# Kernel optimization log

Hardware: AMD Instinct MI355X
Metric: run time of the kernel (lower is better)

## Reference

```python
import jax, jax.numpy as jnp
import numpy as np

B, T, DIM = 2, 2048, 1024
N_HEADS, HEAD_DIM, WINDOW = 16, 64, 512
EPS = 0.01


def _rmsnorm(x, gamma, eps):
    # x: [B, T, H*D] float32; normalize over last dim
    rms = jnp.sqrt(jnp.mean(jnp.square(x), axis=-1, keepdims=True) + eps)
    return x / rms * gamma


def setup_inputs() -> dict:
    key = jax.random.key(0)
    ks = jax.random.split(key, 5)
    s = 1.0 / np.sqrt(DIM)
    return {
        "x": jax.random.normal(ks[0], (B, T, DIM), jnp.float32),
        "wq": jax.random.normal(ks[1], (N_HEADS * HEAD_DIM, DIM), jnp.float32) * s,
        "wk": jax.random.normal(ks[2], (N_HEADS * HEAD_DIM, DIM), jnp.float32) * s,
        "wv": jax.random.normal(ks[3], (N_HEADS * HEAD_DIM, DIM), jnp.float32) * s,
        "wo": jax.random.normal(ks[4], (DIM, N_HEADS * HEAD_DIM), jnp.float32) * s,
        "q_gamma": jnp.ones((N_HEADS * HEAD_DIM,), jnp.float32),
        "k_gamma": jnp.ones((N_HEADS * HEAD_DIM,), jnp.float32),
    }


def reference(x, wq, wk, wv, wo, q_gamma, k_gamma):
    Bx, Tx, _ = x.shape
    H, D = N_HEADS, HEAD_DIM
    # projections (Linear with weight [out,in]): [B,T,H*D]
    q = x @ wq.T
    k = x @ wk.T
    v = (x @ wv.T).reshape(Bx, Tx, H, D).transpose(0, 2, 1, 3)  # [B,H,T,D]
    # QK RMSNorm over the flattened H*D dimension (float32 math)
    q = _rmsnorm(q, q_gamma, 1e-6).reshape(Bx, Tx, H, D).transpose(0, 2, 1, 3)
    k = _rmsnorm(k, k_gamma, 1e-6).reshape(Bx, Tx, H, D).transpose(0, 2, 1, 3)
    scale = 1.0 / np.sqrt(D)
    scores = jnp.einsum("bhqd,bhkd->bhqk", q, k) * scale  # [B,H,T,T]
    # ALiBi bias: slopes[h] * (j - i)
    slopes = jnp.asarray([2.0 ** (-8.0 / H * (h + 1)) for h in range(H)], jnp.float32)
    pos = jnp.arange(Tx)
    dist = (pos[None, :] - pos[:, None]).astype(jnp.float32)  # [T,T], dist[i,j]=j-i
    scores = scores + slopes[None, :, None, None] * dist[None, None]
    # causal (j>i) OR beyond sliding window (i-j > window_size)
    j_minus_i = pos[None, :] - pos[:, None]
    mask = (j_minus_i > 0) | (j_minus_i < -WINDOW)
    scores = jnp.where(mask[None, None], -1e9, scores)
    attn = jax.nn.softmax(scores, axis=-1)
    out = jnp.einsum("bhqk,bhkd->bhqd", attn, v)  # [B,H,T,D]
    out = out.transpose(0, 2, 1, 3).reshape(Bx, Tx, H * D)
    return out @ wo.T
```

## Files before the change

kernel.cpp:

```cpp
#include <hip/hip_runtime.h>
#include <stdint.h>

typedef unsigned short u16;
typedef __bf16 bf16x8 __attribute__((ext_vector_type(8)));
typedef float f32x4 __attribute__((ext_vector_type(4)));

#define MFMA16(a, b, c) __builtin_amdgcn_mfma_f32_16x16x32_bf16((a), (b), (c), 0, 0, 0)

__device__ __forceinline__ u16 f2bf(float f) {
  union { float f; uint32_t u; } v; v.f = f;
  uint32_t r = v.u + 0x7fffu + ((v.u >> 16) & 1u);
  return (u16)(r >> 16);
}
__device__ __forceinline__ float bf2f(u16 h) {
  union { uint32_t u; float f; } v; v.u = ((uint32_t)h) << 16;
  return v.f;
}
__device__ __forceinline__ void gload_lds16(const void* g, void* l) {
  __builtin_amdgcn_global_load_lds(
      (const __attribute__((address_space(1))) uint32_t*)(uintptr_t)g,
      (__attribute__((address_space(3))) uint32_t*)(uintptr_t)l, 16, 0, 0);
}
__device__ __forceinline__ uint32_t cvt_pk_bf16(float a, float b) {
  uint32_t r;
  asm("v_cvt_pk_bf16_f32 %0, %1, %2" : "=v"(r) : "v"(a), "v"(b));
  return r;
}

__global__ void k_cvt_all(const float* __restrict__ x, const float* __restrict__ wq,
                          const float* __restrict__ wk, const float* __restrict__ wv,
                          const float* __restrict__ wo, u16* __restrict__ xb,
                          u16* __restrict__ wqb, u16* __restrict__ wkb, u16* __restrict__ wvb,
                          u16* __restrict__ wob) {
  const int i = blockIdx.x * 256 + threadIdx.x;
  const float* src; u16* dst; int off;
  if (i < 1048576)      { src = x;  dst = xb;  off = i; }
  else if (i < 1310720) { src = wq; dst = wqb; off = i - 1048576; }
  else if (i < 1572864) { src = wk; dst = wkb; off = i - 1310720; }
  else if (i < 1835008) { src = wv; dst = wvb; off = i - 1572864; }
  else                  { src = wo; dst = wob; off = i - 1835008; }
  const float4 v = ((const float4*)src)[off];
  u16 o[4] = { f2bf(v.x), f2bf(v.y), f2bf(v.z), f2bf(v.w) };
  *(uint2*)(dst + 4 * (size_t)off) = *(const uint2*)o;
}

template <bool BF16_OUT, int BN>
__device__ __forceinline__ void gemm_core(const u16* __restrict__ A, const u16* __restrict__ Bw,
                                          void* __restrict__ C, int tm, int tn) {
  constexpr int K = 1024, N = 1024, NT = K / 32;
  constexpr int MF = (BN == 128) ? 4 : 2;
  __shared__ __align__(16) u16 As[2][128 * 32];
  __shared__ __align__(16) u16 Bs[2][BN * 32];
  const int tid = threadIdx.x, l = tid & 63, w = tid >> 6;
  const int wm = (BN == 128) ? (w >> 1) * 64 : w * 32;
  const int wn = (BN == 128) ? (w & 1) * 64 : 0;
  const int lo = l & 15, hi8 = (l >> 4) * 8;
  f32x4 acc[MF][4] = {};

  const int srow = l >> 2, scol = (l & 3) * 8;
  const int c0 = w * 2, c1 = w * 2 + 1;
  const u16* Ag0 = A + (size_t)(tm + c0 * 16 + srow) * K + scol;
  const u16* Ag1 = A + (size_t)(tm + c1 * 16 + srow) * K + scol;
  const u16* Bg0 = Bw + (size_t)(tn + c0 * 16 + srow) * K + scol;
  const u16* Bg1 = Bw + (size_t)(tn + c1 * 16 + srow) * K + scol;
  const u16* BgB = Bw + (size_t)(tn + (tid >> 2)) * K + (tid & 3) * 8;

#define STAGE_G(t, buf)                                  \
  {                                                      \
    const int kt_ = (t) * 32;                            \
    gload_lds16(Ag0 + kt_, &As[(buf)][c0 * 512]);        \
    gload_lds16(Ag1 + kt_, &As[(buf)][c1 * 512]);        \
    if constexpr (BN == 128) {                           \
      gload_lds16(Bg0 + kt_, &Bs[(buf)][c0 * 512]);      \
      gload_lds16(Bg1 + kt_, &Bs[(buf)][c1 * 512]);      \
    } else {                                             \
      gload_lds16(BgB + kt_, &Bs[(buf)][tid * 8]);       \
    }                                                    \
  }

  STAGE_G(0, 0);
  STAGE_G(1, 1);

  for (int t = 0; t < NT; ++t) {
    const int cur = t & 1;
    if (t + 1 < NT) {
      if constexpr (BN == 128) asm volatile("s_waitcnt vmcnt(4)");
      else asm volatile("s_waitcnt vmcnt(3)");
    } else {
      asm volatile("s_waitcnt vmcnt(0)");
    }
    __builtin_amdgcn_s_barrier();
    __builtin_amdgcn_sched_barrier(0);

    bf16x8 af[MF], bfr[4];
#pragma unroll
    for (int m = 0; m < MF; ++m) af[m] = *(const bf16x8*)&As[cur][(wm + m * 16 + lo) * 32 + hi8];
#pragma unroll
    for (int n = 0; n < 4; ++n) bfr[n] = *(const bf16x8*)&Bs[cur][(wn + n * 16 + lo) * 32 + hi8];
#pragma unroll
    for (int m = 0; m < MF; ++m)
#pragma unroll
      for (int n = 0; n < 4; ++n) acc[m][n] = MFMA16(af[m], bfr[n], acc[m][n]);

    __builtin_amdgcn_sched_barrier(0);
    __builtin_amdgcn_s_barrier();
    __builtin_amdgcn_sched_barrier(0);
    if (t + 2 < NT) STAGE_G(t + 2, cur);
  }
#undef STAGE_G

  const int r0 = (l >> 4) * 4;
#pragma unroll
  for (int m = 0; m < MF; ++m)
#pragma unroll
    for (int n = 0; n < 4; ++n)
#pragma unroll
      for (int r = 0; r < 4; ++r) {
        const size_t idx = (size_t)(tm + wm + m * 16 + r0 + r) * N + (tn + wn + n * 16 + lo);
        if (BF16_OUT) ((u16*)C)[idx] = f2bf(acc[m][n][r]);
        else ((float*)C)[idx] = acc[m][n][r];
      }
}

__global__ __launch_bounds__(256, 3) void k_gemm_qkv(
    const u16* __restrict__ X, const u16* __restrict__ Wq, const u16* __restrict__ Wk,
    const u16* __restrict__ Wv, u16* __restrict__ Q, u16* __restrict__ Kt, u16* __restrict__ V) {
  const int n = blockIdx.x + (blockIdx.y << 3) + (blockIdx.z << 8);
  const int wid = (n & 7) * 96 + (n >> 3);
  const int bz = wid >> 8, rem = wid & 255, by = rem >> 3, bx = rem & 7;
  const u16* B = bz == 0 ? Wq : bz == 1 ? Wk : Wv;
  u16* C = bz == 0 ? Q : bz == 1 ? Kt : V;
  gemm_core<true, 128>(X, B, C, by * 128, bx * 128);
}
__global__ __launch_bounds__(256, 4) void k_gemm_out(const u16* __restrict__ Ao,
                                                     const u16* __restrict__ Wo,
                                                     float* __restrict__ C) {
  const int n = blockIdx.x + (blockIdx.y << 4);
  const int wid = (n & 7) * 64 + (n >> 3);
  const int by = wid >> 4, bx = wid & 15;
  gemm_core<false, 64>(Ao, Wo, C, by * 128, bx * 64);
}

__global__ __launch_bounds__(256) void k_rmsnorm(u16* __restrict__ Q, u16* __restrict__ Kt,
                                                 const float* __restrict__ qg,
                                                 const float* __restrict__ kg) {
  const int row = blockIdx.x;
  u16* base = (row < 4096) ? (Q + (size_t)row * 1024) : (Kt + (size_t)(row - 4096) * 1024);
  const float* g = (row < 4096) ? qg : kg;
  const int tid = threadIdx.x;
  ushort4 v = ((const ushort4*)base)[tid];
  float f0 = bf2f(v.x), f1 = bf2f(v.y), f2 = bf2f(v.z), f3 = bf2f(v.w);
  float ss = f0 * f0 + f1 * f1 + f2 * f2 + f3 * f3;
#pragma unroll
  for (int off = 32; off >= 1; off >>= 1) ss += __shfl_xor(ss, off, 64);
  __shared__ float wsum[4];
  if ((tid & 63) == 0) wsum[tid >> 6] = ss;
  __syncthreads();
  ss = wsum[0] + wsum[1] + wsum[2] + wsum[3];
  const float rinv = rsqrtf(ss * (1.0f / 1024.0f) + 1e-6f);
  const float4 gv = ((const float4*)g)[tid];
  v.x = f2bf(f0 * rinv * gv.x);
  v.y = f2bf(f1 * rinv * gv.y);
  v.z = f2bf(f2 * rinv * gv.z);
  v.w = f2bf(f3 * rinv * gv.w);
  ((ushort4*)base)[tid] = v;
}

__global__ __launch_bounds__(512, 4) void k_attn(const u16* __restrict__ Q,
                                                 const u16* __restrict__ Kt,
                                                 const u16* __restrict__ V,
                                                 u16* __restrict__ O) {
  constexpr int T = 2048, HD = 1024, WIN = 512;
  const int nlin = blockIdx.x + (blockIdx.y << 4) + (blockIdx.z << 8);
  const int wid = (nlin & 7) * 64 + (nlin >> 3);
  const int qb = (wid & 15) * 128, h = (wid >> 4) & 15, b = wid >> 8;
  const int tid = threadIdx.x, l = tid & 63, w = tid >> 6;
  const int lo = l & 15, hi = l >> 4;
  const int qw = qb + w * 16;
  const int qg = qw + lo;

  __shared__ __align__(16) u16 Ks[2][64 * 64];
  __shared__ __align__(16) u16 Vt[2][64 * 72];

  const size_t bT = (size_t)b * T;

  bf16x8 qf[2];
  {
    const u16* Qr = Q + (bT + qw + lo) * HD + h * 64 + hi * 8;
    qf[0] = *(const bf16x8*)(Qr);
    qf[1] = *(const bf16x8*)(Qr + 32);
  }

  const int srow = tid >> 3;
  const int kcol = 8 * ((tid & 7) ^ (srow & 7));
  const int vkv = 2 * (l & 31) + (l >> 5);
  const int vd0 = w * 8;
  const u16* Kg0 = Kt + bT * HD + h * 64;
  const u16* Vg0 = V + bT * HD + h * 64;

  float m_r = -1e30f, l_r = 0.f;
  f32x4 o_acc[4] = {};

  const float L2E = 1.4426950408889634f;
  const float scaleL = 0.125f * L2E;
  const float slopeL = exp2f(-0.5f * (float)(h + 1)) * L2E;
  float cn[4], cr[4];
#pragma unroll
  for (int n = 0; n < 4; ++n) cn[n] = slopeL * (float)(n * 16);
#pragma unroll
  for (int r = 0; r < 4; ++r) cr[r] = slopeL * (float)r;

  const int kvs = (qb >= WIN) ? (qb - WIN) : 0;
  const int nt = (qb + 128 - kvs) >> 6;

  {
    const uint4 pkt = *(const uint4*)(Vg0 + (size_t)(kvs + vkv) * HD + vd0);
    gload_lds16(Kg0 + (size_t)(kvs + srow) * HD + kcol, &Ks[0][tid * 8]);
    const u16* e = (const u16*)&pkt;
#pragma unroll
    for (int j = 0; j < 8; ++j) Vt[0][(vd0 + j) * 72 + vkv] = e[j];
  }
  asm volatile("s_waitcnt vmcnt(0)");
  asm volatile("s_waitcnt lgkmcnt(0)");
  __builtin_amdgcn_s_barrier();
  __builtin_amdgcn_sched_barrier(0);

  for (int t = 0; t < nt; ++t) {
    const int kv0 = kvs + t * 64, cur = t & 1;
    const bool pf_next = (t + 1 < nt);
    uint4 vnext;
    if (pf_next) {
      vnext = *(const uint4*)(Vg0 + (size_t)(kv0 + 64 + vkv) * HD + vd0);
      gload_lds16(Kg0 + (size_t)(kv0 + 64 + srow) * HD + kcol, &Ks[cur ^ 1][tid * 8]);
    }

    const bool active = (kv0 <= qw + 15) && (kv0 + 63 + WIN >= qw);
    if (active) {
      f32x4 st[4];
      __builtin_amdgcn_s_setprio(1);
#pragma unroll
      for (int n = 0; n < 4; ++n) {
        f32x4 z = {0.f, 0.f, 0.f, 0.f};
        const int row = n * 16 + lo;
        const int swz = (row & 7) << 4;
#pragma unroll
        for (int kk = 0; kk < 2; ++kk) {
          const bf16x8 kf =
              *(const bf16x8*)((const char*)Ks[cur] + row * 128 + ((kk * 64 + hi * 16) ^ swz));
          z = MFMA16(kf, qf[kk], z);
        }
        st[n] = z;
      }
      __builtin_amdgcn_s_setprio(0);

      const int ddb = kv0 + hi * 4 - qg;
      const float bb = slopeL * (float)ddb;
      float bn[4];
#pragma unroll
      for (int n = 0; n < 4; ++n) bn[n] = bb + cn[n];
      const bool interior = (kv0 + 63 <= qw) && (qw + 15 - kv0 <= WIN);
      if (interior) {
#pragma unroll
        for (int n = 0; n < 4; ++n)
#pragma unroll
          for (int r = 0; r < 4; ++r) st[n][r] = st[n][r] * scaleL + (bn[n] + cr[r]);
      } else {
#pragma unroll
        for (int n = 0; n < 4; ++n)
#pragma unroll
          for (int r = 0; r < 4; ++r) {
            const int dd = ddb + n * 16 + r;
            const float s_ = st[n][r] * scaleL + (bn[n] + cr[r]);
            st[n][r] = (dd > 0 || dd < -WIN) ? -1e30f : s_;
          }
      }

      float mx = -1e30f;
#pragma unroll
      for (int n = 0; n < 4; ++n) {
        const float a = fmaxf(st[n][0], st[n][1]), c = fmaxf(st[n][2], st[n][3]);
        mx = fmaxf(mx, fmaxf(a, c));
      }
      mx = fmaxf(mx, __shfl_xor(mx, 16, 64));
      mx = fmaxf(mx, __shfl_xor(mx, 32, 64));

      float rs = 0.f;
      if (__all(mx - m_r <= 8.0f)) {
#pragma unroll
        for (int n = 0; n < 4; ++n)
#pragma unroll
          for (int r = 0; r < 4; ++r) {
            const float p = exp2f(st[n][r] - m_r);
            st[n][r] = p;
            rs += p;
          }
        rs += __shfl_xor(rs, 16, 64);
        rs += __shfl_xor(rs, 32, 64);
        l_r += rs;
      } else {
        const float mn = fmaxf(m_r, mx);
        const float alpha = exp2f(m_r - mn);
        m_r = mn;
#pragma unroll
        for (int n = 0; n < 4; ++n)
#pragma unroll
          for (int r = 0; r < 4; ++r) {
            const float p = exp2f(st[n][r] - mn);
            st[n][r] = p;
            rs += p;
          }
        rs += __shfl_xor(rs, 16, 64);
        rs += __shfl_xor(rs, 32, 64);
        l_r = l_r * alpha + rs;
#pragma unroll
        for (int nd = 0; nd < 4; ++nd)
#pragma unroll
          for (int r = 0; r < 4; ++r) o_acc[nd][r] *= alpha;
      }

      uint32_t pk[4][2];
#pragma unroll
      for (int n = 0; n < 4; ++n)
#pragma unroll
        for (int d = 0; d < 2; ++d) pk[n][d] = cvt_pk_bf16(st[n][2 * d], st[n][2 * d + 1]);

      uint32_t pfr[2][4];
#pragma unroll
      for (int kk = 0; kk < 2; ++kk)
#pragma unroll
        for (int d = 0; d < 2; ++d) {
          auto s1 = __builtin_amdgcn_permlane32_swap(pk[kk * 2][d], pk[kk * 2 + 1][d], false, false);
          auto s2 = __builtin_amdgcn_permlane16_swap(s1[0], s1[1], false, false);
          pfr[kk][d] = s2[0];
          pfr[kk][2 + d] = s2[1];
        }

      __builtin_amdgcn_s_setprio(1);
#pragma unroll
      for (int kk = 0; kk < 2; ++kk) {
        union { uint32_t u[4]; bf16x8 v; } pu;
#pragma unroll
        for (int d2 = 0; d2 < 4; ++d2) pu.u[d2] = pfr[kk][d2];
        const bf16x8 pv = pu.v;
#pragma unroll
        for (int nd = 0; nd < 4; ++nd) {
          const bf16x8 vf = *(const bf16x8*)&Vt[cur][(nd * 16 + lo) * 72 + kk * 32 + hi * 8];
          o_acc[nd] = MFMA16(vf, pv, o_acc[nd]);
        }
      }
      __builtin_amdgcn_s_setprio(0);
    }

    if (pf_next) {
      const u16* e = (const u16*)&vnext;
#pragma unroll
      for (int j = 0; j < 8; ++j) Vt[cur ^ 1][(vd0 + j) * 72 + vkv] = e[j];
    }
    __builtin_amdgcn_sched_barrier(0);
    asm volatile("s_waitcnt lgkmcnt(0)");
    asm volatile("s_waitcnt vmcnt(0)");
    __builtin_amdgcn_s_barrier();
    __builtin_amdgcn_sched_barrier(0);
  }

  const float inv = 1.f / l_r;
  u16* Og = O + (bT + qw + lo) * HD + h * 64;
#pragma unroll
  for (int nd = 0; nd < 4; ++nd) {
    uint2 pack;
    pack.x = cvt_pk_bf16(o_acc[nd][0] * inv, o_acc[nd][1] * inv);
    pack.y = cvt_pk_bf16(o_acc[nd][2] * inv, o_acc[nd][3] * inv);
    *(uint2*)(Og + nd * 16 + hi * 4) = pack;
  }
}

extern "C" void kernel_launch(void* const* d_in, const int* in_sizes, int n_in,
                              void* d_out, int out_size, void* d_ws, size_t ws_size,
                              hipStream_t stream) {
  const float* x = (const float*)d_in[0];
  const float* wq = (const float*)d_in[1];
  const float* wk = (const float*)d_in[2];
  const float* wv = (const float*)d_in[3];
  const float* wo = (const float*)d_in[4];
  const float* qg = (const float*)d_in[5];
  const float* kg = (const float*)d_in[6];
  float* out = (float*)d_out;

  char* ws = (char*)d_ws;
  const size_t MB = (size_t)1 << 20;
  u16* xb  = (u16*)(ws + 0 * MB);
  u16* wqb = (u16*)(ws + 8 * MB);
  u16* wkb = (u16*)(ws + 10 * MB);
  u16* wvb = (u16*)(ws + 12 * MB);
  u16* wob = (u16*)(ws + 14 * MB);
  u16* qb  = (u16*)(ws + 16 * MB);
  u16* kb  = (u16*)(ws + 24 * MB);
  u16* vb  = (u16*)(ws + 32 * MB);
  u16* ab  = xb;

  k_cvt_all<<<8192, 256, 0, stream>>>(x, wq, wk, wv, wo, xb, wqb, wkb, wvb, wob);
  k_gemm_qkv<<<dim3(8, 32, 3), 256, 0, stream>>>(xb, wqb, wkb, wvb, qb, kb, vb);
  k_rmsnorm<<<8192, 256, 0, stream>>>(qb, kb, qg, kg);
  k_attn<<<dim3(16, 16, 2), 512, 0, stream>>>(qb, kb, vb, ab);
  k_gemm_out<<<dim3(16, 32), 256, 0, stream>>>(ab, wob, out);
}
```

Before: 101.1 us.

## Widen GEMM K-tile to 64 with XOR-swizzled LDS and use permlane reductions

The shared GEMM core now stages 64-wide K slices per iteration instead of 32, halving the loop trip count and barrier count. LDS is written with an XOR swizzle on 16-byte chunks and read back with the matching swizzle to avoid bank conflicts. Launch-bounds occupancy hints are lowered to fit the doubled LDS. The attention softmax row max and row sum reductions replace ds_bpermute-based shuffles with permlane16/32 swap instructions. Lower occupancy may reduce latency hiding.

```diff
diff --git a/kernel.cpp b/kernel.cpp
--- a/kernel.cpp
+++ b/kernel.cpp
@@ -25,6 +25,34 @@
   uint32_t r;
   asm("v_cvt_pk_bf16_f32 %0, %1, %2" : "=v"(r) : "v"(a), "v"(b));
   return r;
+}
+__device__ __forceinline__ float fmax_x16(float x) {
+  union { float f; uint32_t u; } a, b;
+  a.f = x;
+  auto s = __builtin_amdgcn_permlane16_swap(a.u, a.u, false, false);
+  a.u = s[0]; b.u = s[1];
+  return fmaxf(a.f, b.f);
+}
+__device__ __forceinline__ float fmax_x32(float x) {
+  union { float f; uint32_t u; } a, b;
+  a.f = x;
+  auto s = __builtin_amdgcn_permlane32_swap(a.u, a.u, false, false);
+  a.u = s[0]; b.u = s[1];
+  return fmaxf(a.f, b.f);
+}
+__device__ __forceinline__ float fadd_x16(float x) {
+  union { float f; uint32_t u; } a, b;
+  a.f = x;
+  auto s = __builtin_amdgcn_permlane16_swap(a.u, a.u, false, false);
+  a.u = s[0]; b.u = s[1];
+  return a.f + b.f;
+}
+__device__ __forceinline__ float fadd_x32(float x) {
+  union { float f; uint32_t u; } a, b;
+  a.f = x;
+  auto s = __builtin_amdgcn_permlane32_swap(a.u, a.u, false, false);
+  a.u = s[0]; b.u = s[1];
+  return a.f + b.f;
 }
 
 __global__ void k_cvt_all(const float* __restrict__ x, const float* __restrict__ wq,
@@ -47,35 +75,35 @@
 template <bool BF16_OUT, int BN>
 __device__ __forceinline__ void gemm_core(const u16* __restrict__ A, const u16* __restrict__ Bw,
                                           void* __restrict__ C, int tm, int tn) {
-  constexpr int K = 1024, N = 1024, NT = K / 32;
+  constexpr int K = 1024, N = 1024, NT = K / 64;
   constexpr int MF = (BN == 128) ? 4 : 2;
-  __shared__ __align__(16) u16 As[2][128 * 32];
-  __shared__ __align__(16) u16 Bs[2][BN * 32];
+  constexpr int LPS = (BN == 128) ? 8 : 6;
+  __shared__ __align__(16) u16 As[2][128 * 64];
+  __shared__ __align__(16) u16 Bs[2][BN * 64];
   const int tid = threadIdx.x, l = tid & 63, w = tid >> 6;
   const int wm = (BN == 128) ? (w >> 1) * 64 : w * 32;
   const int wn = (BN == 128) ? (w & 1) * 64 : 0;
-  const int lo = l & 15, hi8 = (l >> 4) * 8;
+  const int lo = l & 15, hi = l >> 4;
   f32x4 acc[MF][4] = {};
 
-  const int srow = l >> 2, scol = (l & 3) * 8;
-  const int c0 = w * 2, c1 = w * 2 + 1;
-  const u16* Ag0 = A + (size_t)(tm + c0 * 16 + srow) * K + scol;
-  const u16* Ag1 = A + (size_t)(tm + c1 * 16 + srow) * K + scol;
-  const u16* Bg0 = Bw + (size_t)(tn + c0 * 16 + srow) * K + scol;
-  const u16* Bg1 = Bw + (size_t)(tn + c1 * 16 + srow) * K + scol;
-  const u16* BgB = Bw + (size_t)(tn + (tid >> 2)) * K + (tid & 3) * 8;
-
-#define STAGE_G(t, buf)                                  \
-  {                                                      \
-    const int kt_ = (t) * 32;                            \
-    gload_lds16(Ag0 + kt_, &As[(buf)][c0 * 512]);        \
-    gload_lds16(Ag1 + kt_, &As[(buf)][c1 * 512]);        \
-    if constexpr (BN == 128) {                           \
-      gload_lds16(Bg0 + kt_, &Bs[(buf)][c0 * 512]);      \
-      gload_lds16(Bg1 + kt_, &Bs[(buf)][c1 * 512]);      \
-    } else {                                             \
-      gload_lds16(BgB + kt_, &Bs[(buf)][tid * 8]);       \
-    }                                                    \
+  const int srow = tid >> 3;
+  const int scol = 8 * ((tid & 7) ^ (srow & 7));
+  const u16* Ag = A + (size_t)(tm + srow) * K + scol;
+  const u16* Bg = Bw + (size_t)(tn + srow) * K + scol;
+
+#define STAGE_G(t, buf)                                                     \
+  {                                                                         \
+    const int kt_ = (t) * 64;                                               \
+    gload_lds16(Ag + kt_, &As[(buf)][tid * 8]);                             \
+    gload_lds16(Ag + 32 * K + kt_, &As[(buf)][2048 + tid * 8]);             \
+    gload_lds16(Ag + 64 * K + kt_, &As[(buf)][4096 + tid * 8]);             \
+    gload_lds16(Ag + 96 * K + kt_, &As[(buf)][6144 + tid * 8]);             \
+    gload_lds16(Bg + kt_, &Bs[(buf)][tid * 8]);                             \
+    gload_lds16(Bg + 32 * K + kt_, &Bs[(buf)][2048 + tid * 8]);             \
+    if constexpr (BN == 128) {                                              \
+      gload_lds16(Bg + 64 * K + kt_, &Bs[(buf)][4096 + tid * 8]);           \
+      gload_lds16(Bg + 96 * K + kt_, &Bs[(buf)][6144 + tid * 8]);           \
+    }                                                                       \
   }
 
   STAGE_G(0, 0);
@@ -84,23 +112,34 @@
   for (int t = 0; t < NT; ++t) {
     const int cur = t & 1;
     if (t + 1 < NT) {
-      if constexpr (BN == 128) asm volatile("s_waitcnt vmcnt(4)");
-      else asm volatile("s_waitcnt vmcnt(3)");
+      if constexpr (BN == 128) asm volatile("s_waitcnt vmcnt(8)");
+      else asm volatile("s_waitcnt vmcnt(6)");
     } else {
       asm volatile("s_waitcnt vmcnt(0)");
     }
     __builtin_amdgcn_s_barrier();
     __builtin_amdgcn_sched_barrier(0);
 
-    bf16x8 af[MF], bfr[4];
-#pragma unroll
-    for (int m = 0; m < MF; ++m) af[m] = *(const bf16x8*)&As[cur][(wm + m * 16 + lo) * 32 + hi8];
-#pragma unroll
-    for (int n = 0; n < 4; ++n) bfr[n] = *(const bf16x8*)&Bs[cur][(wn + n * 16 + lo) * 32 + hi8];
-#pragma unroll
-    for (int m = 0; m < MF; ++m)
-#pragma unroll
-      for (int n = 0; n < 4; ++n) acc[m][n] = MFMA16(af[m], bfr[n], acc[m][n]);
+#pragma unroll
+    for (int kk = 0; kk < 2; ++kk) {
+      bf16x8 af[MF], bfr[4];
+#pragma unroll
+      for (int m = 0; m < MF; ++m) {
+        const int row = wm + m * 16 + lo;
+        af[m] = *(const bf16x8*)((const char*)&As[cur][0] + row * 128 +
+                                 ((kk * 64 + hi * 16) ^ ((row & 7) << 4)));
+      }
+#pragma unroll
+      for (int n = 0; n < 4; ++n) {
+        const int row = wn + n * 16 + lo;
+        bfr[n] = *(const bf16x8*)((const char*)&Bs[cur][0] + row * 128 +
+                                  ((kk * 64 + hi * 16) ^ ((row & 7) << 4)));
+      }
+#pragma unroll
+      for (int m = 0; m < MF; ++m)
+#pragma unroll
+        for (int n = 0; n < 4; ++n) acc[m][n] = MFMA16(af[m], bfr[n], acc[m][n]);
+    }
 
     __builtin_amdgcn_sched_barrier(0);
     __builtin_amdgcn_s_barrier();
@@ -122,7 +161,7 @@
       }
 }
 
-__global__ __launch_bounds__(256, 3) void k_gemm_qkv(
+__global__ __launch_bounds__(256, 2) void k_gemm_qkv(
     const u16* __restrict__ X, const u16* __restrict__ Wq, const u16* __restrict__ Wk,
     const u16* __restrict__ Wv, u16* __restrict__ Q, u16* __restrict__ Kt, u16* __restrict__ V) {
   const int n = blockIdx.x + (blockIdx.y << 3) + (blockIdx.z << 8);
@@ -132,7 +171,7 @@
   u16* C = bz == 0 ? Q : bz == 1 ? Kt : V;
   gemm_core<true, 128>(X, B, C, by * 128, bx * 128);
 }
-__global__ __launch_bounds__(256, 4) void k_gemm_out(const u16* __restrict__ Ao,
+__global__ __launch_bounds__(256, 3) void k_gemm_out(const u16* __restrict__ Ao,
                                                      const u16* __restrict__ Wo,
                                                      float* __restrict__ C) {
   const int n = blockIdx.x + (blockIdx.y << 4);
@@ -281,8 +320,7 @@
         const float a = fmaxf(st[n][0], st[n][1]), c = fmaxf(st[n][2], st[n][3]);
         mx = fmaxf(mx, fmaxf(a, c));
       }
-      mx = fmaxf(mx, __shfl_xor(mx, 16, 64));
-      mx = fmaxf(mx, __shfl_xor(mx, 32, 64));
+      mx = fmax_x32(fmax_x16(mx));
 
       float rs = 0.f;
       if (__all(mx - m_r <= 8.0f)) {
@@ -294,8 +332,7 @@
             st[n][r] = p;
             rs += p;
           }
-        rs += __shfl_xor(rs, 16, 64);
-        rs += __shfl_xor(rs, 32, 64);
+        rs = fadd_x32(fadd_x16(rs));
         l_r += rs;
       } else {
         const float mn = fmaxf(m_r, mx);
@@ -309,8 +346,7 @@
             st[n][r] = p;
             rs += p;
           }
-        rs += __shfl_xor(rs, 16, 64);
-        rs += __shfl_xor(rs, 32, 64);
+        rs = fadd_x32(fadd_x16(rs));
         l_r = l_r * alpha + rs;
 #pragma unroll
         for (int nd = 0; nd < 4; ++nd)
```

Result: faster. 95.55 us (-5.5%).
